# Kernel optimization log

Measured on AMD Instinct MI355X. Metric: run time of the kernel, lower is better.

The kernel has to match this reference:

```python
import jax, jax.numpy as jnp
import numpy as np

BN_EPS = 1e-5


def setup_inputs() -> dict:
    key = jax.random.key(0)
    ks = jax.random.split(key, 10)
    d = {}
    # EEG-style input: [B, 1, T, electrodes]
    d["x"] = jax.random.normal(ks[0], (512, 1, 1125, 5), dtype=jnp.float32)
    # conv_time: Conv2d(1, 40, (25, 1)) with bias
    d["conv_time_w"] = jax.random.normal(ks[1], (40, 1, 25, 1), dtype=jnp.float32) * 0.05
    d["conv_time_b"] = jax.random.normal(ks[2], (40,), dtype=jnp.float32) * 0.05
    # conv_spat: Conv2d(40, 40, (1, 5), bias=False)
    d["conv_spat_w"] = jax.random.normal(ks[3], (40, 40, 1, 5), dtype=jnp.float32) * 0.05
    # BatchNorm2d(40), eval mode (running stats)
    d["bn_gamma"] = jnp.ones((40,), jnp.float32)
    d["bn_beta"] = jnp.zeros((40,), jnp.float32)
    d["bn_mean"] = jnp.zeros((40,), jnp.float32)
    d["bn_var"] = jnp.ones((40,), jnp.float32)
    # LSTM(input=40, hidden=10): torch layout W_ih [4H, in], W_hh [4H, H]
    d["w_ih"] = jax.random.normal(ks[4], (40, 40), dtype=jnp.float32) * 0.1
    d["w_hh"] = jax.random.normal(ks[5], (40, 10), dtype=jnp.float32) * 0.1
    d["b_ih"] = jax.random.normal(ks[6], (40,), dtype=jnp.float32) * 0.1
    d["b_hh"] = jax.random.normal(ks[7], (40,), dtype=jnp.float32) * 0.1
    # classifier: Linear(10, 2)
    d["fc_w"] = jax.random.normal(ks[8], (2, 10), dtype=jnp.float32) * 0.1
    d["fc_b"] = jnp.zeros((2,), jnp.float32)
    return d


def reference(x, conv_time_w, conv_time_b, conv_spat_w,
              bn_gamma, bn_beta, bn_mean, bn_var,
              w_ih, w_hh, b_ih, b_hh, fc_w, fc_b):
    dn = ("NCHW", "OIHW", "NCHW")
    # conv over time: [B,1,T,5] -> [B,40,T-24,5]
    h = jax.lax.conv_general_dilated(x, conv_time_w, (1, 1), "VALID", dimension_numbers=dn)
    h = h + conv_time_b[None, :, None, None]
    # conv over electrodes: [B,40,T-24,5] -> [B,40,T-24,1]
    h = jax.lax.conv_general_dilated(h, conv_spat_w, (1, 1), "VALID", dimension_numbers=dn)
    # BatchNorm2d (eval, running stats)
    scale = bn_gamma / jnp.sqrt(bn_var + BN_EPS)
    h = h * scale[None, :, None, None] + (bn_beta - bn_mean * scale)[None, :, None, None]
    # AvgPool2d kernel (25,1) stride (5,1): -> [B,40,L,1], L = (T-24-25)//5 + 1
    h = jax.lax.reduce_window(h, 0.0, jax.lax.add, (1, 1, 25, 1), (1, 1, 5, 1), "VALID") / 25.0
    # Dropout2d in eval mode = identity
    # squeeze width + transpose(1,2): [B,40,L] -> [B,L,40]
    h = jnp.transpose(h[..., 0], (0, 2, 1))
    B = h.shape[0]
    H = w_hh.shape[1]  # hidden = 10
    # precompute input-to-gate projection for all timesteps: [L, B, 4H]
    xg = jnp.einsum("blf,gf->lbg", h, w_ih) + b_ih + b_hh

    def step(carry, xt):
        h_prev, c_prev = carry
        gates = xt + h_prev @ w_hh.T          # [B, 4H]
        i, f, g, o = jnp.split(gates, 4, axis=-1)
        i = jax.nn.sigmoid(i)
        f = jax.nn.sigmoid(f)
        g = jnp.tanh(g)
        o = jax.nn.sigmoid(o)
        c = f * c_prev + i * g
        hn = o * jnp.tanh(c)
        return (hn, c), None

    init = (jnp.zeros((B, H), h.dtype), jnp.zeros((B, H), h.dtype))
    (h_last, _), _ = jax.lax.scan(step, init, xg)  # return_seq=False -> last hidden
    return h_last @ fc_w.T + fc_b  # [B, 2]
```

## Files before the change

kernel.cpp:

```cpp
#include <hip/hip_runtime.h>

#define LOG2E 1.44269504088896340736f

typedef float v2f __attribute__((ext_vector_type(2)));

__device__ __forceinline__ float bf2f(unsigned short u) {
    union { unsigned u32; float f; } v; v.u32 = ((unsigned)u) << 16; return v.f;
}
__device__ __forceinline__ unsigned short f2bf(float f) {
    union { float f; unsigned u32; } v; v.f = f;
    unsigned r = (v.u32 + 0x7FFFu + ((v.u32 >> 16) & 1u)) >> 16;
    return (unsigned short)r;
}
__device__ __forceinline__ bool probe_bf16(const void* gma) {
    return *(const unsigned int*)gma == 0x3F803F80u;
}
__device__ __forceinline__ float ldmix(const void* p, int i, bool bf) {
    return bf ? bf2f(((const unsigned short*)p)[i]) : ((const float*)p)[i];
}
__device__ __forceinline__ float dpp_shl(float x, const int n) {
    int r;
    if (n == 1)      r = __builtin_amdgcn_update_dpp(0, __float_as_int(x), 0x101, 0xF, 0xF, true);
    else if (n == 2) r = __builtin_amdgcn_update_dpp(0, __float_as_int(x), 0x102, 0xF, 0xF, true);
    else             r = __builtin_amdgcn_update_dpp(0, __float_as_int(x), 0x103, 0xF, 0xF, true);
    return __int_as_float(r);
}
#if __has_builtin(__builtin_amdgcn_exp2f)
__device__ __forceinline__ float fexp2(float x) { return __builtin_amdgcn_exp2f(x); }
#else
__device__ __forceinline__ float fexp2(float x) {
    float r; asm("v_exp_f32 %0, %1" : "=v"(r) : "v"(x)); return r;
}
#endif

__global__ __launch_bounds__(1024) void prep_kernel(
    const void* __restrict__ ctw,
    const void* __restrict__ ctb,
    const void* __restrict__ csw,
    const void* __restrict__ gma,
    const void* __restrict__ bta,
    const void* __restrict__ mea,
    const void* __restrict__ var,
    const void* __restrict__ wih,
    const void* __restrict__ bih,
    const void* __restrict__ bhh,
    float* __restrict__ Wg,
    float* __restrict__ Bg)
{
    __shared__ float s_wt[1000];
    __shared__ float s_bt[40];
    __shared__ float s_sp[8000];
    __shared__ float s_wih[1600];
    __shared__ float s_scale[40], s_shift[40];
    __shared__ float s_Wc[5000];
    __shared__ float s_P[5200];
    __shared__ float s_Bc[40];
    __shared__ float s_Wp[9920];

    const int t = threadIdx.x;
    const bool bf = probe_bf16(gma);

    for (int i = t; i < 1000; i += 1024) s_wt[i] = ldmix(ctw, i, bf);
    for (int i = t; i < 8000; i += 1024) s_sp[i] = ldmix(csw, i, bf);
    for (int i = t; i < 1600; i += 1024) s_wih[i] = ldmix(wih, i, bf);
    if (t < 40) {
        s_bt[t] = ldmix(ctb, t, bf);
        float sc = ldmix(gma, t, bf) * rsqrtf(ldmix(var, t, bf) + 1e-5f);
        s_scale[t] = sc;
        s_shift[t] = ldmix(bta, t, bf) - ldmix(mea, t, bf) * sc;
    }
    __syncthreads();

    if (t < 200) {
        const int oc = t / 5, kq = (t % 5) * 5;
        float acc[5][5];
        #pragma unroll
        for (int q = 0; q < 5; ++q)
            #pragma unroll
            for (int e = 0; e < 5; ++e) acc[q][e] = 0.f;
        for (int ic = 0; ic < 40; ++ic) {
            float wtv[5], spv[5];
            #pragma unroll
            for (int q = 0; q < 5; ++q) wtv[q] = s_wt[ic * 25 + kq + q];
            #pragma unroll
            for (int e = 0; e < 5; ++e) spv[e] = s_sp[(oc * 40 + ic) * 5 + e];
            #pragma unroll
            for (int q = 0; q < 5; ++q)
                #pragma unroll
                for (int e = 0; e < 5; ++e) acc[q][e] = fmaf(wtv[q], spv[e], acc[q][e]);
        }
        const float sc = s_scale[oc];
        #pragma unroll
        for (int q = 0; q < 5; ++q)
            #pragma unroll
            for (int e = 0; e < 5; ++e)
                s_Wc[(oc * 25 + kq + q) * 5 + e] = acc[q][e] * sc;
    }
    if (t >= 512 && t < 552) {
        const int oc = t - 512;
        float a = 0.f;
        for (int ic = 0; ic < 40; ++ic) {
            float se = 0.f;
            #pragma unroll
            for (int e = 0; e < 5; ++e) se += s_sp[(oc * 40 + ic) * 5 + e];
            a = fmaf(se, s_bt[ic], a);
        }
        s_Bc[oc] = a * s_scale[oc] + s_shift[oc];
    }
    __syncthreads();

    if (t < 200) {
        const int oc = t / 5, e = t % 5;
        float run = 0.f;
        s_P[oc * 130 + e] = 0.f;
        for (int k = 0; k < 25; ++k) {
            run += s_Wc[(oc * 25 + k) * 5 + e];
            s_P[oc * 130 + (k + 1) * 5 + e] = run;
        }
    }
    __syncthreads();

    for (int i = t; i < 9800; i += 1024) {
        const int oc = i / 245, rem = i % 245, j = rem / 5, e = rem % 5;
        const int lo = j - 24 > 0 ? j - 24 : 0;
        const int hi = j < 24 ? j : 24;
        float val = (s_P[oc * 130 + (hi + 1) * 5 + e] - s_P[oc * 130 + lo * 5 + e]) * 0.04f;
        s_Wp[oc * 248 + rem] = val;
    }
    if (t < 120) s_Wp[(t / 3) * 248 + 245 + (t % 3)] = 0.f;
    __syncthreads();

    if (t < 620) {
        const int gp = t / 31, ko = t % 31;
        const int g0 = 2 * gp, kf0 = 8 * ko;
        float acc0[8], acc1[8];
        #pragma unroll
        for (int q = 0; q < 8; ++q) { acc0[q] = 0.f; acc1[q] = 0.f; }
        for (int oc = 0; oc < 40; ++oc) {
            const float4 pa = *reinterpret_cast<const float4*>(&s_Wp[oc * 248 + kf0]);
            const float4 pb = *reinterpret_cast<const float4*>(&s_Wp[oc * 248 + kf0 + 4]);
            const float wa = s_wih[g0 * 40 + oc];
            const float wb = s_wih[(g0 + 1) * 40 + oc];
            acc0[0] = fmaf(wa, pa.x, acc0[0]); acc0[1] = fmaf(wa, pa.y, acc0[1]);
            acc0[2] = fmaf(wa, pa.z, acc0[2]); acc0[3] = fmaf(wa, pa.w, acc0[3]);
            acc0[4] = fmaf(wa, pb.x, acc0[4]); acc0[5] = fmaf(wa, pb.y, acc0[5]);
            acc0[6] = fmaf(wa, pb.z, acc0[6]); acc0[7] = fmaf(wa, pb.w, acc0[7]);
            acc1[0] = fmaf(wb, pa.x, acc1[0]); acc1[1] = fmaf(wb, pa.y, acc1[1]);
            acc1[2] = fmaf(wb, pa.z, acc1[2]); acc1[3] = fmaf(wb, pa.w, acc1[3]);
            acc1[4] = fmaf(wb, pb.x, acc1[4]); acc1[5] = fmaf(wb, pb.y, acc1[5]);
            acc1[6] = fmaf(wb, pb.z, acc1[6]); acc1[7] = fmaf(wb, pb.w, acc1[7]);
        }
        #pragma unroll
        for (int q = 0; q < 8; ++q) {
            Wg[g0 * 248 + kf0 + q]       = acc0[q];
            Wg[(g0 + 1) * 248 + kf0 + q] = acc1[q];
        }
    }
    if (t >= 640 && t < 680) {
        const int g = t - 640;
        float a = ldmix(bih, g, bf) + ldmix(bhh, g, bf);
        for (int oc = 0; oc < 40; ++oc) a = fmaf(s_wih[g * 40 + oc], s_Bc[oc], a);
        Bg[g] = a;
    }
}

__global__ __launch_bounds__(256, 2) void fused_kernel(
    const void* __restrict__ x,
    const float* __restrict__ Wg,
    const float* __restrict__ Bg,
    const void* __restrict__ whh_p,
    const void* __restrict__ fcw_p,
    const void* __restrict__ fcb_p,
    const void* __restrict__ gma,
    void* __restrict__ out)
{
    __shared__ float sw[9920];
    __shared__ float u[8960];

    const int b   = blockIdx.x;
    const int tid = threadIdx.x;
    const bool bf = probe_bf16(gma);

    for (int i = tid; i < 9920; i += 256) sw[i] = Wg[i];
    if (bf) {
        const unsigned short* xp = (const unsigned short*)x + b * 5625;
        for (int i = tid; i < 5625; i += 256) u[i] = bf2f(xp[i]);
    } else {
        const float* xp = (const float*)x + b * 5625;
        for (int i = tid; i < 5625; i += 256) u[i] = xp[i];
    }
    for (int i = 5625 + tid; i < 6144; i += 256) u[i] = 0.f;
    for (int i = 8640 + tid; i < 8960; i += 256) u[i] = 0.f;
    __syncthreads();

    const int wave  = __builtin_amdgcn_readfirstlane(tid >> 6);
    const int lane  = tid & 63;
    const int gb    = 20 * (wave & 1);
    const int lbase = 108 * (wave >> 1);
    const int l0 = lbase + lane;
    const int l1 = l0 + 64;
    const int a0 = 25 * l0, a1 = 25 * l1;

    v2f acc[20];
    #pragma unroll
    for (int gi = 0; gi < 20; ++gi) {
        float bgv = Bg[gb + gi];
        acc[gi] = (v2f){bgv, bgv};
    }

    const int wrow = gb * 248;
    for (int k = 0; k < 248; k += 4) {
        v2f xv0 = (v2f){ u[a0 + k],     u[a1 + k]     };
        v2f xv1 = (v2f){ u[a0 + k + 1], u[a1 + k + 1] };
        v2f xv2 = (v2f){ u[a0 + k + 2], u[a1 + k + 2] };
        v2f xv3 = (v2f){ u[a0 + k + 3], u[a1 + k + 3] };
        #pragma unroll
        for (int gi = 0; gi < 20; ++gi) {
            const float4 w = *reinterpret_cast<const float4*>(&sw[wrow + gi * 248 + k]);
            acc[gi] += xv0 * w.x;
            acc[gi] += xv1 * w.y;
            acc[gi] += xv2 * w.z;
            acc[gi] += xv3 * w.w;
        }
    }
    __syncthreads();

    #pragma unroll
    for (int gi = 0; gi < 20; ++gi) {
        u[l0 * 40 + gb + gi] = acc[gi].x;
        if (lane < 44) u[l1 * 40 + gb + gi] = acc[gi].y;
    }
    __syncthreads();

    if (wave != 0) return;

    const int j   = lane >> 2;
    const int jt  = lane & 3;
    const int jj  = j < 10 ? j : 9;
    const int gl  = 10 * jt + jj;

    const float L2   = 2.0f * LOG2E;
    const float kmul = (jt == 2) ?  L2 : -LOG2E;
    const float aact = (jt == 2) ? -2.0f : (jt == 0 ? L2 : 1.0f);
    const float bact = (jt == 2) ?  1.0f : 0.0f;

    float whhr[10];
    #pragma unroll
    for (int m = 0; m < 10; ++m) whhr[m] = kmul * ldmix(whh_p, gl * 10 + m, bf);

    float xb[6];
    #pragma unroll
    for (int p = 0; p < 6; ++p) xb[p] = kmul * u[p * 40 + gl];

    float cs = 0.f, h = 0.f;

    for (int l = 0; l < 216; l += 6) {
        #pragma unroll
        for (int s = 0; s < 6; ++s) {
            float xv = xb[s];
            xb[s] = kmul * u[(l + s + 6) * 40 + gl];
            float a_ = xv, b_ = 0.f;
            #pragma unroll
            for (int m = 0; m < 10; m += 2) {
                float h0 = __int_as_float(__builtin_amdgcn_readlane(__float_as_int(h), 4 * m));
                float h1 = __int_as_float(__builtin_amdgcn_readlane(__float_as_int(h), 4 * (m + 1)));
                a_ = fmaf(whhr[m], h0, a_);
                b_ = fmaf(whhr[m + 1], h1, b_);
            }
            float accg = a_ + b_;
            float tt  = fexp2(accg);
            float rr  = __builtin_amdgcn_rcpf(1.0f + tt);
            float act = fmaf(aact, rr, bact);
            float fv = dpp_shl(act, 1);
            float gv = dpp_shl(act, 2);
            float ov = dpp_shl(act, 3);
            cs = fmaf(fv, cs, act * gv);
            float t2 = fexp2(cs);
            float r2 = __builtin_amdgcn_rcpf(1.0f + t2);
            float th = fmaf(-2.0f, r2, 1.0f);
            h = ov * th;
        }
    }

    float w0[10], w1[10];
    #pragma unroll
    for (int m = 0; m < 10; ++m) {
        w0[m] = ldmix(fcw_p, m, bf);
        w1[m] = ldmix(fcw_p, 10 + m, bf);
    }
    float o0 = ldmix(fcb_p, 0, bf), o1 = ldmix(fcb_p, 1, bf);
    #pragma unroll
    for (int m = 0; m < 10; ++m) {
        float hm = __int_as_float(__builtin_amdgcn_readlane(__float_as_int(h), 4 * m));
        o0 = fmaf(w0[m], hm, o0);
        o1 = fmaf(w1[m], hm, o1);
    }
    if (lane == 0) {
        if (bf) {
            ((unsigned short*)out)[b * 2]     = f2bf(o0);
            ((unsigned short*)out)[b * 2 + 1] = f2bf(o1);
        } else {
            ((float*)out)[b * 2]     = o0;
            ((float*)out)[b * 2 + 1] = o1;
        }
    }
}

extern "C" void kernel_launch(void* const* d_in, const int* in_sizes, int n_in,
                              void* d_out, int out_size, void* d_ws, size_t ws_size,
                              hipStream_t stream) {
    const void* x    = d_in[0];
    const void* ctw  = d_in[1];
    const void* ctb  = d_in[2];
    const void* csw  = d_in[3];
    const void* gma  = d_in[4];
    const void* bta  = d_in[5];
    const void* mea  = d_in[6];
    const void* var  = d_in[7];
    const void* wih  = d_in[8];
    const void* whh  = d_in[9];
    const void* bih  = d_in[10];
    const void* bhh  = d_in[11];
    const void* fcw  = d_in[12];
    const void* fcb  = d_in[13];

    char* ws = (char*)d_ws;
    float* Wg = (float*)ws;
    float* Bg = (float*)(ws + 40 * 248 * 4);

    prep_kernel<<<1, 1024, 0, stream>>>(ctw, ctb, csw, gma, bta, mea, var,
                                        wih, bih, bhh, Wg, Bg);
    fused_kernel<<<512, 256, 0, stream>>>(x, Wg, Bg, whh, fcw, fcb, gma, d_out);
}
```

Before: 166.2 us.

## Read projected weights from global in interleaved layout, pad LSTM gate rows

The prep kernel now writes the combined conv/input-projection weights interleaved as [k/4][gate][4], so the fused kernel streams them straight from global/L1 as float4 instead of staging about 40 KB in shared memory. This cuts LDS use per block, which may let more blocks fit on a CU, and drops the staging copy. Gate rows in shared memory get a stride of 41 to avoid bank conflicts. The recurrent dot product is split into four partial sums to shorten the serial dependency chain. The cost is that every weight read now depends on cache hits instead of LDS.

```diff
diff --git a/kernel.cpp b/kernel.cpp
--- a/kernel.cpp
+++ b/kernel.cpp
@@ -24,6 +24,9 @@
     else if (n == 2) r = __builtin_amdgcn_update_dpp(0, __float_as_int(x), 0x102, 0xF, 0xF, true);
     else             r = __builtin_amdgcn_update_dpp(0, __float_as_int(x), 0x103, 0xF, 0xF, true);
     return __int_as_float(r);
+}
+__device__ __forceinline__ float rdlane(float v, int l) {
+    return __int_as_float(__builtin_amdgcn_readlane(__float_as_int(v), l));
 }
 #if __has_builtin(__builtin_amdgcn_exp2f)
 __device__ __forceinline__ float fexp2(float x) { return __builtin_amdgcn_exp2f(x); }
@@ -152,8 +155,10 @@
         }
         #pragma unroll
         for (int q = 0; q < 8; ++q) {
-            Wg[g0 * 248 + kf0 + q]       = acc0[q];
-            Wg[(g0 + 1) * 248 + kf0 + q] = acc1[q];
+            const int kf = kf0 + q;
+            const int base = (kf >> 2) * 160 + (kf & 3);
+            Wg[base + g0 * 4]       = acc0[q];
+            Wg[base + (g0 + 1) * 4] = acc1[q];
         }
     }
     if (t >= 640 && t < 680) {
@@ -174,14 +179,12 @@
     const void* __restrict__ gma,
     void* __restrict__ out)
 {
-    __shared__ float sw[9920];
-    __shared__ float u[8960];
+    __shared__ float u[9216];
 
     const int b   = blockIdx.x;
     const int tid = threadIdx.x;
     const bool bf = probe_bf16(gma);
 
-    for (int i = tid; i < 9920; i += 256) sw[i] = Wg[i];
     if (bf) {
         const unsigned short* xp = (const unsigned short*)x + b * 5625;
         for (int i = tid; i < 5625; i += 256) u[i] = bf2f(xp[i]);
@@ -190,7 +193,7 @@
         for (int i = tid; i < 5625; i += 256) u[i] = xp[i];
     }
     for (int i = 5625 + tid; i < 6144; i += 256) u[i] = 0.f;
-    for (int i = 8640 + tid; i < 8960; i += 256) u[i] = 0.f;
+    for (int i = 8856 + tid; i < 9216; i += 256) u[i] = 0.f;
     __syncthreads();
 
     const int wave  = __builtin_amdgcn_readfirstlane(tid >> 6);
@@ -208,27 +211,32 @@
         acc[gi] = (v2f){bgv, bgv};
     }
 
-    const int wrow = gb * 248;
-    for (int k = 0; k < 248; k += 4) {
+    int dz = 0;
+    asm volatile("" : "+v"(dz));
+    const float4* wq = reinterpret_cast<const float4*>(Wg) + gb + dz;
+
+    for (int k4 = 0; k4 < 62; ++k4) {
+        const int k = 4 * k4;
         v2f xv0 = (v2f){ u[a0 + k],     u[a1 + k]     };
         v2f xv1 = (v2f){ u[a0 + k + 1], u[a1 + k + 1] };
         v2f xv2 = (v2f){ u[a0 + k + 2], u[a1 + k + 2] };
         v2f xv3 = (v2f){ u[a0 + k + 3], u[a1 + k + 3] };
         #pragma unroll
         for (int gi = 0; gi < 20; ++gi) {
-            const float4 w = *reinterpret_cast<const float4*>(&sw[wrow + gi * 248 + k]);
+            const float4 w = wq[gi];
             acc[gi] += xv0 * w.x;
             acc[gi] += xv1 * w.y;
             acc[gi] += xv2 * w.z;
             acc[gi] += xv3 * w.w;
         }
+        wq += 40;
     }
     __syncthreads();
 
     #pragma unroll
     for (int gi = 0; gi < 20; ++gi) {
-        u[l0 * 40 + gb + gi] = acc[gi].x;
-        if (lane < 44) u[l1 * 40 + gb + gi] = acc[gi].y;
+        u[l0 * 41 + gb + gi] = acc[gi].x;
+        if (lane < 44) u[l1 * 41 + gb + gi] = acc[gi].y;
     }
     __syncthreads();
 
@@ -250,7 +258,7 @@
 
     float xb[6];
     #pragma unroll
-    for (int p = 0; p < 6; ++p) xb[p] = kmul * u[p * 40 + gl];
+    for (int p = 0; p < 6; ++p) xb[p] = kmul * u[p * 41 + gl];
 
     float cs = 0.f, h = 0.f;
 
@@ -258,16 +266,22 @@
         #pragma unroll
         for (int s = 0; s < 6; ++s) {
             float xv = xb[s];
-            xb[s] = kmul * u[(l + s + 6) * 40 + gl];
-            float a_ = xv, b_ = 0.f;
-            #pragma unroll
-            for (int m = 0; m < 10; m += 2) {
-                float h0 = __int_as_float(__builtin_amdgcn_readlane(__float_as_int(h), 4 * m));
-                float h1 = __int_as_float(__builtin_amdgcn_readlane(__float_as_int(h), 4 * (m + 1)));
-                a_ = fmaf(whhr[m], h0, a_);
-                b_ = fmaf(whhr[m + 1], h1, b_);
-            }
-            float accg = a_ + b_;
+            xb[s] = kmul * u[(l + s + 6) * 41 + gl];
+            float h0 = rdlane(h, 0),  h1 = rdlane(h, 4),  h2 = rdlane(h, 8);
+            float h3 = rdlane(h, 12), h4 = rdlane(h, 16), h5 = rdlane(h, 20);
+            float h6 = rdlane(h, 24), h7 = rdlane(h, 28), h8 = rdlane(h, 32);
+            float h9 = rdlane(h, 36);
+            float p0 = fmaf(whhr[0], h0, xv);
+            float p1 = whhr[1] * h1;
+            float p2 = whhr[2] * h2;
+            float p3 = whhr[3] * h3;
+            p0 = fmaf(whhr[4], h4, p0);
+            p1 = fmaf(whhr[5], h5, p1);
+            p2 = fmaf(whhr[6], h6, p2);
+            p3 = fmaf(whhr[7], h7, p3);
+            p0 = fmaf(whhr[8], h8, p0);
+            p1 = fmaf(whhr[9], h9, p1);
+            float accg = (p0 + p2) + (p1 + p3);
             float tt  = fexp2(accg);
             float rr  = __builtin_amdgcn_rcpf(1.0f + tt);
             float act = fmaf(aact, rr, bact);
@@ -291,7 +305,7 @@
     float o0 = ldmix(fcb_p, 0, bf), o1 = ldmix(fcb_p, 1, bf);
     #pragma unroll
     for (int m = 0; m < 10; ++m) {
-        float hm = __int_as_float(__builtin_amdgcn_readlane(__float_as_int(h), 4 * m));
+        float hm = rdlane(h, 4 * m);
         o0 = fmaf(w0[m], hm, o0);
         o1 = fmaf(w1[m], hm, o1);
     }
```

Measured after the change: 196.6 us. 1.18x slower.
